# Performance work log

Measured on AMD Instinct MI355X. Metric: run time of the kernel, lower is better.

The kernel has to match this reference:

```python
import jax, jax.numpy as jnp
import numpy as np

B, S, D = 2, 2048, 1024
H = 16
HD = D // H  # 64


def setup_inputs() -> dict:
    key = jax.random.key(0)
    k1, k2, k3, k4, k5, k6 = jax.random.split(key, 6)
    hidden_states = jax.random.normal(k1, (B, S, D), dtype=jnp.float32)
    attention_mask = jax.random.randint(k2, (B, S), 0, 2, dtype=jnp.int32)
    scale = 1.0 / np.sqrt(D)
    Wq = jax.random.normal(k3, (D, D), dtype=jnp.float32) * scale
    bq = jax.random.normal(k4, (D,), dtype=jnp.float32) * 0.02
    Wk = jax.random.normal(k5, (D, D), dtype=jnp.float32) * scale
    bk = jax.random.normal(k6, (D,), dtype=jnp.float32) * 0.02
    return {"hidden_states": hidden_states, "attention_mask": attention_mask,
            "Wq": Wq, "bq": bq, "Wk": Wk, "bk": bk}


def _split_heads(x):
    # [B, S, D] -> [B, H, S, HD]
    b, s, _ = x.shape
    return x.reshape(b, s, H, HD).transpose(0, 2, 1, 3)


def reference(hidden_states, attention_mask, Wq, bq, Wk, bk):
    dh = jnp.sqrt(jnp.float32(HD))
    q = _split_heads(hidden_states @ Wq + bq)            # [B,H,S,HD]
    k = _split_heads(hidden_states @ Wk + bk)            # [B,H,S,HD]
    v = q + k                                            # value = Q + K
    k_t = -jax.nn.log_sigmoid(-k)                        # negate the logsigmoid(-K) transform
    scores = jnp.einsum('bhqd,bhkd->bhqk', q, k_t) / dh  # [B,H,S,S]
    # mask applied on the QUERY axis (dim 2), broadcast over key axis (faithful to source)
    mask = (attention_mask[:, None, :, None] == 0)       # [B,1,S,1]
    scores = jnp.where(mask, jnp.float32(-10000.0), scores)
    probs = jax.nn.softmax(scores, axis=-1)              # dropout: eval mode (identity)
    ctx = jnp.einsum('bhqk,bhkd->bhqd', probs, v)        # [B,H,S,HD]
    ctx = ctx.transpose(0, 2, 1, 3).reshape(B, S, D)
    return ctx
```

## Files before the change

### kernel.cpp

```cpp
#include <hip/hip_runtime.h>
#include <hip/hip_bf16.h>

#define B_ 2
#define S_ 2048
#define D_ 1024
#define H_ 16
#define HD_ 64

typedef __attribute__((ext_vector_type(8))) short short8;
typedef __attribute__((ext_vector_type(4))) short short4v;
typedef __attribute__((ext_vector_type(4))) float float4v;

typedef const __attribute__((address_space(1))) void* gas_ptr;
typedef __attribute__((address_space(3))) void* las_ptr;

static __device__ inline void gl_lds16(const void* g, void* l) {
  __builtin_amdgcn_global_load_lds((gas_ptr)g, (las_ptr)l, 16, 0, 0);
}

static __device__ inline short f2bs(float x) {
  __hip_bfloat16 h = __float2bfloat16(x);
  union { __hip_bfloat16 h; short s; } u; u.h = h; return u.s;
}
static __device__ inline float bs2f(short s) {
  union { short s; __hip_bfloat16 h; } u; u.s = s; return __bfloat162float(u.h);
}
static __device__ inline short4v pk4(float a, float b, float c, float d) {
  union { __hip_bfloat162 h[2]; short4v s; } u;
  u.h[0] = __float22bfloat162_rn(float2{a, b});
  u.h[1] = __float22bfloat162_rn(float2{c, d});
  return u.s;
}

static __device__ inline float4v mfma32(short8 a, short8 b, float4v c) {
  return __builtin_amdgcn_mfma_f32_16x16x32_bf16(a, b, c, 0, 0, 0);
}
static __device__ inline float4v mfma16(short4v a, short4v b, float4v c) {
  return __builtin_amdgcn_mfma_f32_16x16x16bf16_1k(a, b, c, 0, 0, 0);
}

__global__ __launch_bounds__(256) void prep(
    const float* __restrict__ hs, __hip_bfloat16* __restrict__ hsb,
    const float* __restrict__ Wq, const float* __restrict__ Wk,
    __hip_bfloat16* __restrict__ Wqt, __hip_bfloat16* __restrict__ Wkt) {
  __shared__ float t[64][65];
  const int id = blockIdx.x;
  if (id < 2048) {
    const size_t i = ((size_t)id * 256 + threadIdx.x) * 8;
    const float4v a0 = ((const float4v*)(hs + i))[0];
    const float4v a1 = ((const float4v*)(hs + i))[1];
    short8 s;
#pragma unroll
    for (int j = 0; j < 4; ++j) { s[j] = f2bs(a0[j]); s[4 + j] = f2bs(a1[j]); }
    *(short8*)(hsb + i) = s;
    return;
  }
  const int bid = id - 2048;
  const float* W = (bid >> 8) ? Wk : Wq;
  __hip_bfloat16* Wt = (bid >> 8) ? Wkt : Wqt;
  const int n0 = (bid & 15) * 64, k0 = ((bid >> 4) & 15) * 64;
  const int c = threadIdx.x & 63, r0 = threadIdx.x >> 6;
  for (int i = 0; i < 16; ++i) {
    const int r = i * 4 + r0;
    t[c][r] = W[(size_t)(k0 + r) * D_ + n0 + c];
  }
  __syncthreads();
  for (int i = 0; i < 16; ++i) {
    const int rr = i * 4 + r0;
    Wt[(size_t)(n0 + rr) * D_ + k0 + c] = __float2bfloat16(t[rr][c]);
  }
}

__global__ __launch_bounds__(256, 2) void gemm_fused(
    const __hip_bfloat16* __restrict__ hsb,
    const __hip_bfloat16* __restrict__ Wqt, const __hip_bfloat16* __restrict__ Wkt,
    const float* __restrict__ bq, const float* __restrict__ bk,
    __hip_bfloat16* __restrict__ q_out, __hip_bfloat16* __restrict__ kt_out,
    __hip_bfloat16* __restrict__ vT) {
  const int id = blockIdx.x;
  const int mt = (id & 7) * 8 + ((id >> 3) & 7);
  const int nt = id >> 6;
  const int n0 = nt * 128, m0 = mt * 64;
  __shared__ __hip_bfloat16 As[2][64 * 32];
  __shared__ __hip_bfloat16 Bq[2][128 * 32];
  __shared__ __hip_bfloat16 Bk[2][128 * 32];
  const int tid = threadIdx.x, wid = tid >> 6, lane = tid & 63;
  const int wm = (wid >> 1) * 32, wn = (wid & 1) * 64;
  const int l15 = lane & 15, l4 = lane >> 4;
  const float4v zz = {0.f, 0.f, 0.f, 0.f};
  float4v accq[2][4], acck[2][4];
  for (int i = 0; i < 2; ++i)
    for (int j = 0; j < 4; ++j) { accq[i][j] = zz; acck[i][j] = zz; }
  const int lrow = wid * 16 + (lane >> 2);
  const int lk8 = (((lane & 3) ^ ((lane >> 3) & 3)) * 8);
  {
    gl_lds16(hsb + (size_t)(m0 + lrow) * D_ + lk8, As[0] + wid * 512);
    gl_lds16(Wqt + (size_t)(n0 + lrow) * D_ + lk8, Bq[0] + wid * 512);
    gl_lds16(Wqt + (size_t)(n0 + 64 + lrow) * D_ + lk8, Bq[0] + 2048 + wid * 512);
    gl_lds16(Wkt + (size_t)(n0 + lrow) * D_ + lk8, Bk[0] + wid * 512);
    gl_lds16(Wkt + (size_t)(n0 + 64 + lrow) * D_ + lk8, Bk[0] + 2048 + wid * 512);
  }
  int p = 0;
  for (int kb = 0; kb < 32; ++kb) {
    __syncthreads();
    if (kb < 31) {
      const int kc = (kb + 1) * 32 + lk8;
      gl_lds16(hsb + (size_t)(m0 + lrow) * D_ + kc, As[p ^ 1] + wid * 512);
      gl_lds16(Wqt + (size_t)(n0 + lrow) * D_ + kc, Bq[p ^ 1] + wid * 512);
      gl_lds16(Wqt + (size_t)(n0 + 64 + lrow) * D_ + kc, Bq[p ^ 1] + 2048 + wid * 512);
      gl_lds16(Wkt + (size_t)(n0 + lrow) * D_ + kc, Bk[p ^ 1] + wid * 512);
      gl_lds16(Wkt + (size_t)(n0 + 64 + lrow) * D_ + kc, Bk[p ^ 1] + 2048 + wid * 512);
    }
    short8 af[2], bfq[4], bfk[4];
    const int fo = ((l4 ^ ((l15 >> 1) & 3)) * 8);
    for (int rt = 0; rt < 2; ++rt)
      af[rt] = *(const short8*)(As[p] + (wm + rt * 16 + l15) * 32 + fo);
    for (int ct = 0; ct < 4; ++ct) {
      bfq[ct] = *(const short8*)(Bq[p] + (wn + ct * 16 + l15) * 32 + fo);
      bfk[ct] = *(const short8*)(Bk[p] + (wn + ct * 16 + l15) * 32 + fo);
    }
    for (int rt = 0; rt < 2; ++rt)
      for (int ct = 0; ct < 4; ++ct) {
        accq[rt][ct] = mfma32(af[rt], bfq[ct], accq[rt][ct]);
        acck[rt][ct] = mfma32(af[rt], bfk[ct], acck[rt][ct]);
      }
    p ^= 1;
  }
  float bvq[4], bvk[4];
  for (int ct = 0; ct < 4; ++ct) {
    bvq[ct] = bq[n0 + wn + ct * 16 + l15];
    bvk[ct] = bk[n0 + wn + ct * 16 + l15];
  }
  for (int rt = 0; rt < 2; ++rt)
    for (int ct = 0; ct < 4; ++ct) {
      const int col = n0 + wn + ct * 16 + l15;
      const int h = col >> 6, d = col & 63;
      const int rowb = m0 + wm + rt * 16 + l4 * 4;
      short4v vv;
      for (int r = 0; r < 4; ++r) {
        const int row = rowb + r;
        const float qv = accq[rt][ct][r] + bvq[ct];
        const float kv = acck[rt][ct][r] + bvk[ct];
        const float sp = fmaxf(kv, 0.f) + __logf(1.f + __expf(-fabsf(kv)));
        q_out[(size_t)row * D_ + col] = __float2bfloat16(qv);
        kt_out[(size_t)row * D_ + col] = __float2bfloat16(sp);
        vv[r] = f2bs(qv + kv);
      }
      const int b = rowb >> 11, s = rowb & 2047;
      const int sw = (s & ~63) | (((s >> 4) & 3) << 2) | (((s >> 2) & 3) << 4);
      *(short4v*)(vT + ((size_t)(b * H_ + h) * HD_ + d) * S_ + sw) = vv;
    }
}

__global__ __launch_bounds__(256, 4) void attn(
    const __hip_bfloat16* __restrict__ qb, const __hip_bfloat16* __restrict__ ktb,
    const __hip_bfloat16* __restrict__ vT, const int* __restrict__ mask,
    float* __restrict__ po, float* __restrict__ pl) {
  __shared__ short smem[17408];
  const int id = blockIdx.x;
  const int xcd = id & 7;
  const int rest = id >> 3;
  const int qt = rest & 15;
  const int kr = (rest >> 4) & 1;
  const int hb = (rest >> 5) * 8 + xcd;
  const int h = hb >> 1, b = hb & 1;
  const int q0 = qt * 128;
  const int k0 = kr * 1024;
  const int pid = hb * 16 + qt;
  const int tid = threadIdx.x, wid = tid >> 6, lane = tid & 63;
  const int l15 = lane & 15, l4 = lane >> 4;
  const int qs = wid * 32;
  const __hip_bfloat16* qh = qb + (size_t)b * S_ * D_ + h * HD_;
  const __hip_bfloat16* kh_ = ktb + (size_t)b * S_ * D_ + h * HD_;
  const __hip_bfloat16* vh = vT + (size_t)(b * H_ + h) * HD_ * S_;
  const int srow = tid >> 2;
  const int b0 = tid & 3;
  const int ssw = ((srow & 1) << 2) | ((srow >> 1) & 3);
  const int w0 = srow * 64 + ((b0 ^ ssw) * 8);
  const int w1 = srow * 64 + (((b0 + 4) ^ ssw) * 8);

  const float SC = 0.125f * 1.44269504f;
  short8 bq0[2], bq1[2];
#pragma unroll
  for (int T = 0; T < 2; ++T) {
    const int qr = q0 + qs + T * 16 + l15;
    const float mq = (mask[b * S_ + qr] != 0) ? SC : 0.f;
    const short8 r0 = *(const short8*)(qh + (size_t)qr * D_ + l4 * 8);
    const short8 r1 = *(const short8*)(qh + (size_t)qr * D_ + 32 + l4 * 8);
#pragma unroll
    for (int j = 0; j < 8; ++j) {
      bq0[T][j] = f2bs(bs2f(r0[j]) * mq);
      bq1[T][j] = f2bs(bs2f(r1[j]) * mq);
    }
  }

  const int lsw = ((l15 & 1) << 2) | ((l15 >> 1) & 3);
  const int ak0off = l15 * 64 + ((l4 ^ lsw) * 8);
  const int ak1off = l15 * 64 + (((l4 + 4) ^ lsw) * 8);
  const int vb0off = ((2 * l4) ^ lsw) * 8;
  const int vb1off = ((2 * l4 + 1) ^ lsw) * 8;

  const float4v zz = {0.f, 0.f, 0.f, 0.f};
  float4v oacc[2][4];
#pragma unroll
  for (int T = 0; T < 2; ++T)
#pragma unroll
    for (int dt = 0; dt < 4; ++dt) oacc[T][dt] = zz;
  float4v ls[2] = {zz, zz};

  short8 gk0, gk1, gv0, gv1;
  gk0 = *(const short8*)(kh_ + (size_t)(k0 + srow) * D_ + b0 * 8);
  gk1 = *(const short8*)(kh_ + (size_t)(k0 + srow) * D_ + b0 * 8 + 32);
  gv0 = *(const short8*)(vh + (size_t)srow * S_ + k0 + b0 * 8);
  gv1 = *(const short8*)(vh + (size_t)srow * S_ + k0 + b0 * 8 + 32);

  int pb = 0;
  for (int c = 0; c < 16; ++c) {
    short* bufp = smem + pb * 8192;
    *(short8*)(bufp + w0) = gk0;
    *(short8*)(bufp + w1) = gk1;
    *(short8*)(bufp + 4096 + w0) = gv0;
    *(short8*)(bufp + 4096 + w1) = gv1;
    __syncthreads();
    if (c < 15) {
      const int kb = k0 + (c + 1) * 64;
      gk0 = *(const short8*)(kh_ + (size_t)(kb + srow) * D_ + b0 * 8);
      gk1 = *(const short8*)(kh_ + (size_t)(kb + srow) * D_ + b0 * 8 + 32);
      gv0 = *(const short8*)(vh + (size_t)srow * S_ + kb + b0 * 8);
      gv1 = *(const short8*)(vh + (size_t)srow * S_ + kb + b0 * 8 + 32);
    }
    const short* kbase = bufp;
    const short* vbase = bufp + 4096;
    short4v pf[2][4];
#pragma unroll
    for (int t = 0; t < 4; ++t) {
      const short8 ak0 = *(const short8*)(kbase + t * 1024 + ak0off);
      const short8 ak1 = *(const short8*)(kbase + t * 1024 + ak1off);
#pragma unroll
      for (int T = 0; T < 2; ++T) {
        float4v cc = zz;
        cc = mfma32(ak0, bq0[T], cc);
        cc = mfma32(ak1, bq1[T], cc);
        float e[4];
#pragma unroll
        for (int r = 0; r < 4; ++r) {
          e[r] = __builtin_amdgcn_exp2f(cc[r]); ls[T][r] += e[r];
        }
        pf[T][t] = pk4(e[0], e[1], e[2], e[3]);
      }
    }
#pragma unroll
    for (int dt = 0; dt < 4; ++dt) {
      const int rb = (dt * 16 + l15) * 64;
      const short8 av0 = *(const short8*)(vbase + rb + vb0off);
      const short8 av1 = *(const short8*)(vbase + rb + vb1off);
      const short4v a0 = {av0[0], av0[1], av0[2], av0[3]};
      const short4v a1 = {av0[4], av0[5], av0[6], av0[7]};
      const short4v a2 = {av1[0], av1[1], av1[2], av1[3]};
      const short4v a3 = {av1[4], av1[5], av1[6], av1[7]};
#pragma unroll
      for (int T = 0; T < 2; ++T) {
        oacc[T][dt] = mfma16(a0, pf[T][0], oacc[T][dt]);
        oacc[T][dt] = mfma16(a1, pf[T][1], oacc[T][dt]);
        oacc[T][dt] = mfma16(a2, pf[T][2], oacc[T][dt]);
        oacc[T][dt] = mfma16(a3, pf[T][3], oacc[T][dt]);
      }
    }
    pb ^= 1;
  }
  float lT[2];
#pragma unroll
  for (int T = 0; T < 2; ++T) {
    lT[T] = (ls[T][0] + ls[T][1]) + (ls[T][2] + ls[T][3]);
    lT[T] += __shfl_xor(lT[T], 16);
    lT[T] += __shfl_xor(lT[T], 32);
  }
  __syncthreads();
  float* mbuf = (float*)smem;
#pragma unroll
  for (int T = 0; T < 2; ++T) {
    const int row = qs + T * 16 + l15;
#pragma unroll
    for (int dt = 0; dt < 4; ++dt)
      *(float4v*)&mbuf[row * 68 + dt * 16 + l4 * 4] = oacc[T][dt];
    if (l4 == 0) pl[(size_t)(kr * 512 + pid) * 128 + row] = lT[T];
  }
  __syncthreads();
  float* pbase = po + (size_t)(kr * 512 + pid) * 8192 + qs * 64;
#pragma unroll
  for (int i = 0; i < 8; ++i) {
    const int e = i * 256 + lane * 4;
    const int row = qs + (e >> 6), col = e & 63;
    *(float4v*)(pbase + e) = *(const float4v*)&mbuf[row * 68 + col];
  }
}

__global__ __launch_bounds__(256) void comb(
    const float* __restrict__ po, const float* __restrict__ pl,
    float* __restrict__ out) {
  const int pid = blockIdx.x;
  const int t = threadIdx.x;
  const int qt = pid & 15, hb = pid >> 4;
  const int h = hb >> 1, bb = hb & 1;
  const float* p0 = po + (size_t)pid * 8192;
  const float* p1 = po + (size_t)(512 + pid) * 8192;
  const float* l0 = pl + (size_t)pid * 128;
  const float* l1 = pl + (size_t)(512 + pid) * 128;
#pragma unroll
  for (int i = 0; i < 8; ++i) {
    const int e = i * 1024 + t * 4;
    const int row = e >> 6, col = e & 63;
    float4v a = *(const float4v*)(p0 + e);
    const float4v bv = *(const float4v*)(p1 + e);
    const float li = 1.f / (l0[row] + l1[row]);
#pragma unroll
    for (int r = 0; r < 4; ++r) a[r] = (a[r] + bv[r]) * li;
    *(float4v*)(out + (size_t)(bb * S_ + qt * 128 + row) * D_ + h * HD_ + col) = a;
  }
}

extern "C" void kernel_launch(void* const* d_in, const int* in_sizes, int n_in,
                              void* d_out, int out_size, void* d_ws, size_t ws_size,
                              hipStream_t stream) {
  const float* hs = (const float*)d_in[0];
  const int* mask = (const int*)d_in[1];
  const float* Wq = (const float*)d_in[2];
  const float* bq = (const float*)d_in[3];
  const float* Wk = (const float*)d_in[4];
  const float* bk = (const float*)d_in[5];
  float* out = (float*)d_out;
  char* ws = (char*)d_ws;
  const size_t MB = 1u << 20;
  __hip_bfloat16* q_b = (__hip_bfloat16*)(ws + 0 * MB);
  __hip_bfloat16* k_b = (__hip_bfloat16*)(ws + 8 * MB);
  __hip_bfloat16* vT  = (__hip_bfloat16*)(ws + 16 * MB);
  __hip_bfloat16* Wqt = (__hip_bfloat16*)(ws + 24 * MB);
  __hip_bfloat16* Wkt = (__hip_bfloat16*)(ws + 26 * MB);
  __hip_bfloat16* hsb = (__hip_bfloat16*)(ws + 28 * MB);
  float* po = (float*)(ws + 24 * MB);
  float* pl = (float*)(ws + 56 * MB);

  prep<<<dim3(2560), 256, 0, stream>>>(hs, hsb, Wq, Wk, Wqt, Wkt);
  gemm_fused<<<dim3(512), 256, 0, stream>>>(hsb, Wqt, Wkt, bq, bk, q_b, k_b, vT);
  attn<<<dim3(1024), 256, 0, stream>>>(q_b, k_b, vT, mask, po, pl);
  comb<<<dim3(512), 256, 0, stream>>>(po, pl, out);
}
```

Measured before the change: 166.9 us.

## Drop split-K attention and combine kernel; load K/V straight from global memory

The two-way key split and the separate combine kernel are removed. Each attention block now walks all 2048 keys and normalizes its output directly into the final tensor, which avoids writing and re-reading the partial output and row-sum buffers. K and V fragments are loaded from global memory into registers per wave, with no LDS double buffering and no barriers. The PV product now uses the 16x16x32 MFMA with packed probability fragments. The trade-offs are half as many blocks (lower occupancy hint) and redundant, unprefetched global loads across the four waves of a block, which leave more memory latency exposed.

```diff
diff --git a/kernel.cpp b/kernel.cpp
--- a/kernel.cpp
+++ b/kernel.cpp
@@ -25,18 +25,17 @@
 static __device__ inline float bs2f(short s) {
   union { short s; __hip_bfloat16 h; } u; u.s = s; return __bfloat162float(u.h);
 }
-static __device__ inline short4v pk4(float a, float b, float c, float d) {
-  union { __hip_bfloat162 h[2]; short4v s; } u;
-  u.h[0] = __float22bfloat162_rn(float2{a, b});
-  u.h[1] = __float22bfloat162_rn(float2{c, d});
+static __device__ inline short8 pk8(const float* a, const float* b) {
+  union { __hip_bfloat162 h[4]; short8 s; } u;
+  u.h[0] = __float22bfloat162_rn(float2{a[0], a[1]});
+  u.h[1] = __float22bfloat162_rn(float2{a[2], a[3]});
+  u.h[2] = __float22bfloat162_rn(float2{b[0], b[1]});
+  u.h[3] = __float22bfloat162_rn(float2{b[2], b[3]});
   return u.s;
 }
 
 static __device__ inline float4v mfma32(short8 a, short8 b, float4v c) {
   return __builtin_amdgcn_mfma_f32_16x16x32_bf16(a, b, c, 0, 0, 0);
-}
-static __device__ inline float4v mfma16(short4v a, short4v b, float4v c) {
-  return __builtin_amdgcn_mfma_f32_16x16x16bf16_1k(a, b, c, 0, 0, 0);
 }
 
 __global__ __launch_bounds__(256) void prep(
@@ -152,32 +151,24 @@
     }
 }
 
-__global__ __launch_bounds__(256, 4) void attn(
+__global__ __launch_bounds__(256, 2) void attn(
     const __hip_bfloat16* __restrict__ qb, const __hip_bfloat16* __restrict__ ktb,
     const __hip_bfloat16* __restrict__ vT, const int* __restrict__ mask,
-    float* __restrict__ po, float* __restrict__ pl) {
-  __shared__ short smem[17408];
+    float* __restrict__ out) {
+  __shared__ float mbuf[128 * 68 + 128];
   const int id = blockIdx.x;
   const int xcd = id & 7;
   const int rest = id >> 3;
   const int qt = rest & 15;
-  const int kr = (rest >> 4) & 1;
-  const int hb = (rest >> 5) * 8 + xcd;
+  const int hb = (rest >> 4) * 8 + xcd;
   const int h = hb >> 1, b = hb & 1;
   const int q0 = qt * 128;
-  const int k0 = kr * 1024;
-  const int pid = hb * 16 + qt;
   const int tid = threadIdx.x, wid = tid >> 6, lane = tid & 63;
   const int l15 = lane & 15, l4 = lane >> 4;
   const int qs = wid * 32;
   const __hip_bfloat16* qh = qb + (size_t)b * S_ * D_ + h * HD_;
-  const __hip_bfloat16* kh_ = ktb + (size_t)b * S_ * D_ + h * HD_;
+  const __hip_bfloat16* kh = ktb + (size_t)b * S_ * D_ + h * HD_;
   const __hip_bfloat16* vh = vT + (size_t)(b * H_ + h) * HD_ * S_;
-  const int srow = tid >> 2;
-  const int b0 = tid & 3;
-  const int ssw = ((srow & 1) << 2) | ((srow >> 1) & 3);
-  const int w0 = srow * 64 + ((b0 ^ ssw) * 8);
-  const int w1 = srow * 64 + (((b0 + 4) ^ ssw) * 8);
 
   const float SC = 0.125f * 1.44269504f;
   short8 bq0[2], bq1[2];
@@ -194,12 +185,6 @@
     }
   }
 
-  const int lsw = ((l15 & 1) << 2) | ((l15 >> 1) & 3);
-  const int ak0off = l15 * 64 + ((l4 ^ lsw) * 8);
-  const int ak1off = l15 * 64 + (((l4 + 4) ^ lsw) * 8);
-  const int vb0off = ((2 * l4) ^ lsw) * 8;
-  const int vb1off = ((2 * l4 + 1) ^ lsw) * 8;
-
   const float4v zz = {0.f, 0.f, 0.f, 0.f};
   float4v oacc[2][4];
 #pragma unroll
@@ -208,65 +193,62 @@
     for (int dt = 0; dt < 4; ++dt) oacc[T][dt] = zz;
   float4v ls[2] = {zz, zz};
 
-  short8 gk0, gk1, gv0, gv1;
-  gk0 = *(const short8*)(kh_ + (size_t)(k0 + srow) * D_ + b0 * 8);
-  gk1 = *(const short8*)(kh_ + (size_t)(k0 + srow) * D_ + b0 * 8 + 32);
-  gv0 = *(const short8*)(vh + (size_t)srow * S_ + k0 + b0 * 8);
-  gv1 = *(const short8*)(vh + (size_t)srow * S_ + k0 + b0 * 8 + 32);
-
-  int pb = 0;
-  for (int c = 0; c < 16; ++c) {
-    short* bufp = smem + pb * 8192;
-    *(short8*)(bufp + w0) = gk0;
-    *(short8*)(bufp + w1) = gk1;
-    *(short8*)(bufp + 4096 + w0) = gv0;
-    *(short8*)(bufp + 4096 + w1) = gv1;
-    __syncthreads();
-    if (c < 15) {
-      const int kb = k0 + (c + 1) * 64;
-      gk0 = *(const short8*)(kh_ + (size_t)(kb + srow) * D_ + b0 * 8);
-      gk1 = *(const short8*)(kh_ + (size_t)(kb + srow) * D_ + b0 * 8 + 32);
-      gv0 = *(const short8*)(vh + (size_t)srow * S_ + kb + b0 * 8);
-      gv1 = *(const short8*)(vh + (size_t)srow * S_ + kb + b0 * 8 + 32);
-    }
-    const short* kbase = bufp;
-    const short* vbase = bufp + 4096;
-    short4v pf[2][4];
+  const __hip_bfloat16* kbase = kh + (size_t)l15 * D_ + l4 * 8;
+  const __hip_bfloat16* vbase = vh + (size_t)l15 * S_ + l4 * 16;
+
+  for (int c = 0; c < 32; ++c) {
+    const int k0 = c * 64;
+    short8 ck0[4], ck1[4], cv0[4], cv1[4];
 #pragma unroll
     for (int t = 0; t < 4; ++t) {
-      const short8 ak0 = *(const short8*)(kbase + t * 1024 + ak0off);
-      const short8 ak1 = *(const short8*)(kbase + t * 1024 + ak1off);
+      const __hip_bfloat16* kp = kbase + (size_t)(k0 + t * 16) * D_;
+      ck0[t] = *(const short8*)(kp);
+      ck1[t] = *(const short8*)(kp + 32);
+    }
+#pragma unroll
+    for (int dt = 0; dt < 4; ++dt) {
+      const __hip_bfloat16* vp = vbase + (size_t)(dt * 16) * S_ + k0;
+      cv0[dt] = *(const short8*)(vp);
+      cv1[dt] = *(const short8*)(vp + 8);
+    }
+    short8 p01[2], p23[2];
+#pragma unroll
+    for (int T = 0; T < 2; ++T) {
+      float e0[4], e1[4], e2[4], e3[4];
+      {
+        float4v cc = mfma32(ck0[0], bq0[T], zz);
+        cc = mfma32(ck1[0], bq1[T], cc);
+#pragma unroll
+        for (int r = 0; r < 4; ++r) { e0[r] = __builtin_amdgcn_exp2f(cc[r]); ls[T][r] += e0[r]; }
+      }
+      {
+        float4v cc = mfma32(ck0[1], bq0[T], zz);
+        cc = mfma32(ck1[1], bq1[T], cc);
+#pragma unroll
+        for (int r = 0; r < 4; ++r) { e1[r] = __builtin_amdgcn_exp2f(cc[r]); ls[T][r] += e1[r]; }
+      }
+      {
+        float4v cc = mfma32(ck0[2], bq0[T], zz);
+        cc = mfma32(ck1[2], bq1[T], cc);
+#pragma unroll
+        for (int r = 0; r < 4; ++r) { e2[r] = __builtin_amdgcn_exp2f(cc[r]); ls[T][r] += e2[r]; }
+      }
+      {
+        float4v cc = mfma32(ck0[3], bq0[T], zz);
+        cc = mfma32(ck1[3], bq1[T], cc);
+#pragma unroll
+        for (int r = 0; r < 4; ++r) { e3[r] = __builtin_amdgcn_exp2f(cc[r]); ls[T][r] += e3[r]; }
+      }
+      p01[T] = pk8(e0, e1);
+      p23[T] = pk8(e2, e3);
+    }
+#pragma unroll
+    for (int dt = 0; dt < 4; ++dt)
 #pragma unroll
       for (int T = 0; T < 2; ++T) {
-        float4v cc = zz;
-        cc = mfma32(ak0, bq0[T], cc);
-        cc = mfma32(ak1, bq1[T], cc);
-        float e[4];
-#pragma unroll
-        for (int r = 0; r < 4; ++r) {
-          e[r] = __builtin_amdgcn_exp2f(cc[r]); ls[T][r] += e[r];
-        }
-        pf[T][t] = pk4(e[0], e[1], e[2], e[3]);
-      }
-    }
-#pragma unroll
-    for (int dt = 0; dt < 4; ++dt) {
-      const int rb = (dt * 16 + l15) * 64;
-      const short8 av0 = *(const short8*)(vbase + rb + vb0off);
-      const short8 av1 = *(const short8*)(vbase + rb + vb1off);
-      const short4v a0 = {av0[0], av0[1], av0[2], av0[3]};
-      const short4v a1 = {av0[4], av0[5], av0[6], av0[7]};
-      const short4v a2 = {av1[0], av1[1], av1[2], av1[3]};
-      const short4v a3 = {av1[4], av1[5], av1[6], av1[7]};
-#pragma unroll
-      for (int T = 0; T < 2; ++T) {
-        oacc[T][dt] = mfma16(a0, pf[T][0], oacc[T][dt]);
-        oacc[T][dt] = mfma16(a1, pf[T][1], oacc[T][dt]);
-        oacc[T][dt] = mfma16(a2, pf[T][2], oacc[T][dt]);
-        oacc[T][dt] = mfma16(a3, pf[T][3], oacc[T][dt]);
-      }
-    }
-    pb ^= 1;
+        oacc[T][dt] = mfma32(cv0[dt], p01[T], oacc[T][dt]);
+        oacc[T][dt] = mfma32(cv1[dt], p23[T], oacc[T][dt]);
+      }
   }
   float lT[2];
 #pragma unroll
@@ -275,47 +257,26 @@
     lT[T] += __shfl_xor(lT[T], 16);
     lT[T] += __shfl_xor(lT[T], 32);
   }
-  __syncthreads();
-  float* mbuf = (float*)smem;
+  float* ml = mbuf + 128 * 68;
 #pragma unroll
   for (int T = 0; T < 2; ++T) {
     const int row = qs + T * 16 + l15;
 #pragma unroll
     for (int dt = 0; dt < 4; ++dt)
       *(float4v*)&mbuf[row * 68 + dt * 16 + l4 * 4] = oacc[T][dt];
-    if (l4 == 0) pl[(size_t)(kr * 512 + pid) * 128 + row] = lT[T];
+    if (l4 == 0) ml[row] = lT[T];
   }
   __syncthreads();
-  float* pbase = po + (size_t)(kr * 512 + pid) * 8192 + qs * 64;
+  const int qq = tid & 127;
+  const int dg = (tid >> 7) * 32;
+  const float li = 1.f / ml[qq];
+  float* orow = out + (size_t)(b * S_ + q0 + qq) * D_ + h * HD_ + dg;
 #pragma unroll
   for (int i = 0; i < 8; ++i) {
-    const int e = i * 256 + lane * 4;
-    const int row = qs + (e >> 6), col = e & 63;
-    *(float4v*)(pbase + e) = *(const float4v*)&mbuf[row * 68 + col];
-  }
-}
-
-__global__ __launch_bounds__(256) void comb(
-    const float* __restrict__ po, const float* __restrict__ pl,
-    float* __restrict__ out) {
-  const int pid = blockIdx.x;
-  const int t = threadIdx.x;
-  const int qt = pid & 15, hb = pid >> 4;
-  const int h = hb >> 1, bb = hb & 1;
-  const float* p0 = po + (size_t)pid * 8192;
-  const float* p1 = po + (size_t)(512 + pid) * 8192;
-  const float* l0 = pl + (size_t)pid * 128;
-  const float* l1 = pl + (size_t)(512 + pid) * 128;
-#pragma unroll
-  for (int i = 0; i < 8; ++i) {
-    const int e = i * 1024 + t * 4;
-    const int row = e >> 6, col = e & 63;
-    float4v a = *(const float4v*)(p0 + e);
-    const float4v bv = *(const float4v*)(p1 + e);
-    const float li = 1.f / (l0[row] + l1[row]);
-#pragma unroll
-    for (int r = 0; r < 4; ++r) a[r] = (a[r] + bv[r]) * li;
-    *(float4v*)(out + (size_t)(bb * S_ + qt * 128 + row) * D_ + h * HD_ + col) = a;
+    float4v v = *(const float4v*)&mbuf[qq * 68 + dg + i * 4];
+#pragma unroll
+    for (int r = 0; r < 4; ++r) v[r] *= li;
+    *(float4v*)(orow + i * 4) = v;
   }
 }
 
@@ -337,11 +298,8 @@
   __hip_bfloat16* Wqt = (__hip_bfloat16*)(ws + 24 * MB);
   __hip_bfloat16* Wkt = (__hip_bfloat16*)(ws + 26 * MB);
   __hip_bfloat16* hsb = (__hip_bfloat16*)(ws + 28 * MB);
-  float* po = (float*)(ws + 24 * MB);
-  float* pl = (float*)(ws + 56 * MB);
 
   prep<<<dim3(2560), 256, 0, stream>>>(hs, hsb, Wq, Wk, Wqt, Wkt);
   gemm_fused<<<dim3(512), 256, 0, stream>>>(hsb, Wqt, Wkt, bq, bk, q_b, k_b, vT);
-  attn<<<dim3(1024), 256, 0, stream>>>(q_b, k_b, vT, mask, po, pl);
-  comb<<<dim3(512), 256, 0, stream>>>(po, pl, out);
-}
+  attn<<<dim3(512), 256, 0, stream>>>(q_b, k_b, vT, mask, out);
+}
```

Result: slower. 233.5 us (+39.9%).
